# Performance work log

Hardware: AMD Instinct MI355X
Metric: run time of the kernel (lower is better)

Reference implementation:

```python
import jax, jax.numpy as jnp
import numpy as np

OUT, IN, RANK = 4096, 4096, 256
SUBVEC = 8
N_SUBVECS = OUT * RANK // SUBVEC  # 131072 (same for Vh since IN == OUT here)
NNZ = 262144


def setup_inputs() -> dict:
    key = jax.random.key(0)
    ks = jax.random.split(key, 8)
    x = jax.random.normal(ks[0], (4, 128, IN), dtype=jnp.float32)
    U_indices = jax.random.randint(ks[1], (N_SUBVECS,), 0, 256, dtype=jnp.int32)
    U_codebook = jax.random.normal(ks[2], (256, SUBVEC), dtype=jnp.float32)
    S = jax.random.uniform(ks[3], (RANK,), dtype=jnp.float32)
    Vh_indices = jax.random.randint(ks[4], (N_SUBVECS,), 0, 256, dtype=jnp.int32)
    Vh_codebook = jax.random.normal(ks[5], (256, SUBVEC), dtype=jnp.float32)
    residual_indices = jax.random.randint(ks[6], (NNZ,), 0, OUT * IN, dtype=jnp.int32)
    residual_values = jax.random.normal(ks[7], (NNZ,), dtype=jnp.float32)
    return {
        "x": x,
        "U_indices": U_indices,
        "U_codebook": U_codebook,
        "S": S,
        "Vh_indices": Vh_indices,
        "Vh_codebook": Vh_codebook,
        "residual_indices": residual_indices,
        "residual_values": residual_values,
    }


def reference(x, U_indices, U_codebook, S, Vh_indices, Vh_codebook,
              residual_indices, residual_values):
    # Codebook gather -> flatten -> reshape to factor shape (dims divide evenly,
    # so torch's flat[:n] truncation is a no-op here).
    U = U_codebook[U_indices].reshape(OUT, RANK)      # [out, rank]
    Vh = Vh_codebook[Vh_indices].reshape(RANK, IN)    # [rank, in]
    # U @ diag(S) @ Vh, fused as column-scale of U
    weight = (U * S[None, :]) @ Vh                    # [out, in]
    # sparse residual scatter-add into the flat weight
    weight = weight.reshape(-1).at[residual_indices].add(residual_values)
    weight = weight.reshape(OUT, IN)
    # F.linear(x, weight) == x @ weight.T (bias is None)
    return jnp.einsum("bsi,oi->bso", x, weight)
```

## Files before the change

### kernel.cpp

```cpp
#include <hip/hip_runtime.h>
#include <hip/hip_bf16.h>
#include <stdint.h>

#define IN_DIM   4096
#define OUT_DIM  4096
#define RANK     256
#define MROWS    512
#define NNZ_CNT  262144
#define BCAP     128
#define CSTRIDE  16

typedef __attribute__((ext_vector_type(8))) short bf16x8;
typedef __attribute__((ext_vector_type(4))) float f32x4;

#define WS_VHB  ((size_t)0)
#define WS_USB  (WS_VHB + (size_t)RANK * IN_DIM * 2)
#define WS_XT   (WS_USB + (size_t)OUT_DIM * RANK * 2)
#define WS_T    (WS_XT  + (size_t)IN_DIM * MROWS * 2)
#define WS_CUR  (WS_T   + (size_t)MROWS * RANK * 4)
#define WS_KVB  (WS_CUR + (size_t)OUT_DIM * CSTRIDE * 4)

__device__ inline uint4 pack8(float4 a, float4 b) {
    union { __hip_bfloat16 h[8]; uint4 u; } w;
    w.h[0] = __float2bfloat16(a.x); w.h[1] = __float2bfloat16(a.y);
    w.h[2] = __float2bfloat16(a.z); w.h[3] = __float2bfloat16(a.w);
    w.h[4] = __float2bfloat16(b.x); w.h[5] = __float2bfloat16(b.y);
    w.h[6] = __float2bfloat16(b.z); w.h[7] = __float2bfloat16(b.w);
    return w.u;
}

__device__ inline float bfbits(uint32_t lo16) {
    union { uint32_t u; float f; } w; w.u = lo16 << 16; return w.f;
}

__device__ inline void fma8(float* acc, uint4 u, float v) {
    acc[0] += v * bfbits(u.x & 0xffffu);
    acc[1] += v * bfbits(u.x >> 16);
    acc[2] += v * bfbits(u.y & 0xffffu);
    acc[3] += v * bfbits(u.y >> 16);
    acc[4] += v * bfbits(u.z & 0xffffu);
    acc[5] += v * bfbits(u.z >> 16);
    acc[6] += v * bfbits(u.w & 0xffffu);
    acc[7] += v * bfbits(u.w >> 16);
}

__global__ __launch_bounds__(256) void prep_kernel(
    const float* __restrict__ x,
    const int*   __restrict__ uidx, const float* __restrict__ ucode,
    const float* __restrict__ S,
    const int*   __restrict__ vidx, const float* __restrict__ vcode,
    __hip_bfloat16* __restrict__ Vhb, __hip_bfloat16* __restrict__ Usb,
    __hip_bfloat16* __restrict__ xT,
    int* __restrict__ cursor, float* __restrict__ tbuf)
{
    const int bid = blockIdx.x;
    const int t   = threadIdx.x;

    if (bid < 512) {
        __shared__ float tile[64][65];
        const int i0 = (bid >> 3) * 64;
        const int m0 = (bid & 7) * 64;
        const int rr = t >> 4, c4 = t & 15;
        #pragma unroll
        for (int p = 0; p < 4; p++) {
            int r = p * 16 + rr;
            float4 v = *(const float4*)(x + (size_t)(m0 + r) * IN_DIM + i0 + c4 * 4);
            tile[r][c4 * 4 + 0] = v.x;
            tile[r][c4 * 4 + 1] = v.y;
            tile[r][c4 * 4 + 2] = v.z;
            tile[r][c4 * 4 + 3] = v.w;
        }
        tbuf[bid * 256 + t] = 0.f;
        __syncthreads();
        #pragma unroll
        for (int p = 0; p < 4; p++) {
            int i = p * 16 + rr;
            union { __hip_bfloat16 h[4]; uint2 u; } w;
            w.h[0] = __float2bfloat16(tile[c4 * 4 + 0][i]);
            w.h[1] = __float2bfloat16(tile[c4 * 4 + 1][i]);
            w.h[2] = __float2bfloat16(tile[c4 * 4 + 2][i]);
            w.h[3] = __float2bfloat16(tile[c4 * 4 + 3][i]);
            *(uint2*)(xT + (size_t)(i0 + i) * MROWS + m0 + c4 * 4) = w.u;
        }
    } else if (bid < 768) {
        int base = (bid - 512) * 512;
        #pragma unroll
        for (int q = 0; q < 2; q++) {
            int sv = base + q * 256 + t;
            int cb = vidx[sv];
            const float4* vc = (const float4*)(vcode + (size_t)cb * 8);
            *(uint4*)(Vhb + (size_t)sv * 8) = pack8(vc[0], vc[1]);
        }
    } else {
        int base = (bid - 768) * 512;
        #pragma unroll
        for (int q = 0; q < 2; q++) {
            int sv = base + q * 256 + t;
            int cb = uidx[sv];
            int r0 = (sv & 31) * 8;
            const float4* uc = (const float4*)(ucode + (size_t)cb * 8);
            const float4* sp = (const float4*)(S + r0);
            float4 a = uc[0], b = uc[1], sa = sp[0], sb = sp[1];
            a.x *= sa.x; a.y *= sa.y; a.z *= sa.z; a.w *= sa.w;
            b.x *= sb.x; b.y *= sb.y; b.z *= sb.z; b.w *= sb.w;
            *(uint4*)(Usb + (size_t)sv * 8) = pack8(a, b);
        }
        cursor[(bid - 768) * 256 + t] = 0;
    }
}

__global__ __launch_bounds__(256) void scatter_gemm1_kernel(
    const int* __restrict__ ridx, const float* __restrict__ rval,
    int* __restrict__ cursor, int2* __restrict__ kvb,
    const float* __restrict__ x,
    const __hip_bfloat16* __restrict__ Vhb,
    float* __restrict__ tbuf)
{
    if (blockIdx.x < 1024) {
        int k = blockIdx.x * 256 + threadIdx.x;
        int idx = ridx[k];
        int o = idx >> 12, i = idx & 4095;
        int pos = atomicAdd(&cursor[o * CSTRIDE], 1);
        if (pos < BCAP)
            kvb[(size_t)o * BCAP + pos] = make_int2(i, __float_as_int(rval[k]));
        return;
    }

    __shared__ __align__(16) __hip_bfloat16 As[64][72];
    __shared__ __align__(16) __hip_bfloat16 Bs[64][72];

    const int bid = blockIdx.x - 1024;
    const int ks = bid & 7, nb = (bid >> 3) & 3, mb = bid >> 5;
    const int m0 = mb * 64, n0 = nb * 64, kbase = ks * 512;
    const int t = threadIdx.x;
    const int lane = t & 63, wave = t >> 6;
    const int wm = wave >> 1, wn = wave & 1;
    const int l15 = lane & 15, l4 = lane >> 4;
    const int srow = t >> 2, sg = t & 3;

    f32x4 acc[2][2];
    #pragma unroll
    for (int i = 0; i < 2; i++)
        #pragma unroll
        for (int j = 0; j < 2; j++) acc[i][j] = (f32x4){0.f, 0.f, 0.f, 0.f};

    for (int s = 0; s < 8; s++) {
        int k0 = kbase + s * 64;
        const float* xp = x + (size_t)(m0 + srow) * IN_DIM + k0 + sg * 16;
        *(uint4*)&As[srow][sg * 16] =
            pack8(*(const float4*)xp, *(const float4*)(xp + 4));
        *(uint4*)&As[srow][sg * 16 + 8] =
            pack8(*(const float4*)(xp + 8), *(const float4*)(xp + 12));
        const __hip_bfloat16* bp = Vhb + (size_t)(n0 + srow) * IN_DIM + k0 + sg * 16;
        *(uint4*)&Bs[srow][sg * 16]     = *(const uint4*)bp;
        *(uint4*)&Bs[srow][sg * 16 + 8] = *(const uint4*)(bp + 8);
        __syncthreads();
        #pragma unroll
        for (int kk = 0; kk < 2; kk++) {
            bf16x8 a[2], b[2];
            #pragma unroll
            for (int i = 0; i < 2; i++)
                a[i] = *(const bf16x8*)&As[wm * 32 + i * 16 + l15][kk * 32 + l4 * 8];
            #pragma unroll
            for (int j = 0; j < 2; j++)
                b[j] = *(const bf16x8*)&Bs[wn * 32 + j * 16 + l15][kk * 32 + l4 * 8];
            #pragma unroll
            for (int i = 0; i < 2; i++)
                #pragma unroll
                for (int j = 0; j < 2; j++)
                    acc[i][j] = __builtin_amdgcn_mfma_f32_16x16x32_bf16(
                        a[i], b[j], acc[i][j], 0, 0, 0);
        }
        __syncthreads();
    }

    #pragma unroll
    for (int i = 0; i < 2; i++)
        #pragma unroll
        for (int j = 0; j < 2; j++)
            #pragma unroll
            for (int q = 0; q < 4; q++) {
                int row = m0 + wm * 32 + i * 16 + l4 * 4 + q;
                int col = n0 + wn * 32 + j * 16 + l15;
                atomicAdd(&tbuf[row * RANK + col], acc[i][j][q]);
            }
}

__global__ __launch_bounds__(256) void gemm2_sparse_kernel(
    const float* __restrict__ tbuf,
    const __hip_bfloat16* __restrict__ Usb,
    const int* __restrict__ cursor,
    const int2* __restrict__ kvb,
    const __hip_bfloat16* __restrict__ xT,
    float* __restrict__ out)
{
    __shared__ __align__(16) char smem[14080];
    typedef __hip_bfloat16 bfrowA[72];
    typedef __hip_bfloat16 bfrowB[72];
    bfrowA* As = (bfrowA*)smem;
    bfrowB* Bs = (bfrowB*)(smem + 4608);
    float (*sacc)[33] = (float(*)[33])smem;

    const int bid = blockIdx.x;
    const int mb = bid & 15, nb = bid >> 4;
    const int m0 = mb * 32, n0 = nb * 64;
    const int t = threadIdx.x;
    const int lane = t & 63, wave = t >> 6;
    const int wm = wave >> 1, wn = wave & 1;
    const int l15 = lane & 15, l4 = lane >> 4;

    f32x4 acc[2];
    acc[0] = (f32x4){0.f, 0.f, 0.f, 0.f};
    acc[1] = (f32x4){0.f, 0.f, 0.f, 0.f};

    {
        const int sa_row = t >> 3, sa_g = t & 7;
        const int sb_row = t >> 2, sb_g = t & 3;
        for (int s = 0; s < 4; s++) {
            int k0 = s * 64;
            const float* tp = tbuf + (size_t)(m0 + sa_row) * RANK + k0 + sa_g * 8;
            *(uint4*)&As[sa_row][sa_g * 8] =
                pack8(*(const float4*)tp, *(const float4*)(tp + 4));
            const __hip_bfloat16* bp =
                Usb + (size_t)(n0 + sb_row) * RANK + k0 + sb_g * 16;
            *(uint4*)&Bs[sb_row][sb_g * 16]     = *(const uint4*)bp;
            *(uint4*)&Bs[sb_row][sb_g * 16 + 8] = *(const uint4*)(bp + 8);
            __syncthreads();
            #pragma unroll
            for (int kk = 0; kk < 2; kk++) {
                bf16x8 a, b[2];
                a = *(const bf16x8*)&As[wm * 16 + l15][kk * 32 + l4 * 8];
                #pragma unroll
                for (int j = 0; j < 2; j++)
                    b[j] = *(const bf16x8*)&Bs[wn * 32 + j * 16 + l15][kk * 32 + l4 * 8];
                #pragma unroll
                for (int j = 0; j < 2; j++)
                    acc[j] = __builtin_amdgcn_mfma_f32_16x16x32_bf16(
                        a, b[j], acc[j], 0, 0, 0);
            }
            __syncthreads();
        }
    }

    {
        const int orel = t >> 2;
        const int ms   = t & 3;
        const int o    = n0 + orel;
        int cnt = cursor[o * CSTRIDE]; cnt = cnt < BCAP ? cnt : BCAP;
        const int2* kp  = kvb + (size_t)o * BCAP;
        const int4* kp4 = (const int4*)kp;
        const __hip_bfloat16* xm = xT + m0 + ms * 8;

        float r[8];
        #pragma unroll
        for (int j = 0; j < 8; j++) r[j] = 0.f;

        int k = 0;
        for (; k + 8 <= cnt; k += 8) {
            int4 e0 = kp4[(k >> 1) + 0], e1 = kp4[(k >> 1) + 1];
            int4 e2 = kp4[(k >> 1) + 2], e3 = kp4[(k >> 1) + 3];
            uint4 u0 = *(const uint4*)(xm + (size_t)e0.x * MROWS);
            uint4 u1 = *(const uint4*)(xm + (size_t)e0.z * MROWS);
            uint4 u2 = *(const uint4*)(xm + (size_t)e1.x * MROWS);
            uint4 u3 = *(const uint4*)(xm + (size_t)e1.z * MROWS);
            uint4 u4 = *(const uint4*)(xm + (size_t)e2.x * MROWS);
            uint4 u5 = *(const uint4*)(xm + (size_t)e2.z * MROWS);
            uint4 u6 = *(const uint4*)(xm + (size_t)e3.x * MROWS);
            uint4 u7 = *(const uint4*)(xm + (size_t)e3.z * MROWS);
            fma8(r, u0, __int_as_float(e0.y));
            fma8(r, u1, __int_as_float(e0.w));
            fma8(r, u2, __int_as_float(e1.y));
            fma8(r, u3, __int_as_float(e1.w));
            fma8(r, u4, __int_as_float(e2.y));
            fma8(r, u5, __int_as_float(e2.w));
            fma8(r, u6, __int_as_float(e3.y));
            fma8(r, u7, __int_as_float(e3.w));
        }
        if (k + 4 <= cnt) {
            int4 e0 = kp4[(k >> 1) + 0], e1 = kp4[(k >> 1) + 1];
            uint4 u0 = *(const uint4*)(xm + (size_t)e0.x * MROWS);
            uint4 u1 = *(const uint4*)(xm + (size_t)e0.z * MROWS);
            uint4 u2 = *(const uint4*)(xm + (size_t)e1.x * MROWS);
            uint4 u3 = *(const uint4*)(xm + (size_t)e1.z * MROWS);
            fma8(r, u0, __int_as_float(e0.y));
            fma8(r, u1, __int_as_float(e0.w));
            fma8(r, u2, __int_as_float(e1.y));
            fma8(r, u3, __int_as_float(e1.w));
            k += 4;
        }
        for (; k < cnt; k++) {
            int2 e = kp[k];
            uint4 u = *(const uint4*)(xm + (size_t)e.x * MROWS);
            fma8(r, u, __int_as_float(e.y));
        }

        *(float4*)&sacc[orel][ms * 8]     = make_float4(r[0], r[1], r[2], r[3]);
        *(float4*)&sacc[orel][ms * 8 + 4] = make_float4(r[4], r[5], r[6], r[7]);
    }
    __syncthreads();

    #pragma unroll
    for (int j = 0; j < 2; j++)
        #pragma unroll
        for (int q = 0; q < 4; q++) {
            int rrel = wm * 16 + l4 * 4 + q;
            int crel = wn * 32 + j * 16 + l15;
            out[(size_t)(m0 + rrel) * OUT_DIM + n0 + crel] =
                acc[j][q] + sacc[crel][rrel];
        }
}

extern "C" void kernel_launch(void* const* d_in, const int* in_sizes, int n_in,
                              void* d_out, int out_size, void* d_ws, size_t ws_size,
                              hipStream_t stream)
{
    const float* x    = (const float*)d_in[0];
    const int*   uidx = (const int*)  d_in[1];
    const float* ucb  = (const float*)d_in[2];
    const float* S    = (const float*)d_in[3];
    const int*   vidx = (const int*)  d_in[4];
    const float* vcb  = (const float*)d_in[5];
    const int*   ridx = (const int*)  d_in[6];
    const float* rval = (const float*)d_in[7];
    float* out = (float*)d_out;

    char* ws = (char*)d_ws;
    __hip_bfloat16* Vhb  = (__hip_bfloat16*)(ws + WS_VHB);
    __hip_bfloat16* Usb  = (__hip_bfloat16*)(ws + WS_USB);
    __hip_bfloat16* xT   = (__hip_bfloat16*)(ws + WS_XT);
    float*          tbuf = (float*)(ws + WS_T);
    int*            cur  = (int*)(ws + WS_CUR);
    int2*           kvb  = (int2*)(ws + WS_KVB);

    prep_kernel<<<dim3(1024), dim3(256), 0, stream>>>(
        x, uidx, ucb, S, vidx, vcb, Vhb, Usb, xT, cur, tbuf);

    scatter_gemm1_kernel<<<dim3(1280), dim3(256), 0, stream>>>(
        ridx, rval, cur, kvb, x, Vhb, tbuf);

    gemm2_sparse_kernel<<<dim3(1024), dim3(256), 0, stream>>>(
        tbuf, Usb, cur, kvb, xT, out);
}
```

Before: 62.69 us.

## Double gemm2 block threads, split sparse nonzero lists across two halves

The gemm2_sparse kernel moves from 256 to 512 threads per block. The A and B tile loads are split between the two halves of the block, and each wave now computes one 16x16 MFMA tile instead of two. Each output column's sparse residual list is split between two threads whose partial sums are combined through an enlarged shared-memory buffer. This aims to raise parallelism and memory-level concurrency in the latency-bound sparse gather, at the cost of more shared memory, more threads and shorter unrolled gather loops.

Result: slower. 65.29 us (+4.2%).

```diff
diff --git a/kernel.cpp b/kernel.cpp
--- a/kernel.cpp
+++ b/kernel.cpp
@@ -186,7 +186,7 @@
             }
 }
 
-__global__ __launch_bounds__(256) void gemm2_sparse_kernel(
+__global__ __launch_bounds__(512, 8) void gemm2_sparse_kernel(
     const float* __restrict__ tbuf,
     const __hip_bfloat16* __restrict__ Usb,
     const int* __restrict__ cursor,
@@ -194,59 +194,58 @@
     const __hip_bfloat16* __restrict__ xT,
     float* __restrict__ out)
 {
-    __shared__ __align__(16) char smem[14080];
+    __shared__ __align__(16) char smem[16896];
     typedef __hip_bfloat16 bfrowA[72];
     typedef __hip_bfloat16 bfrowB[72];
     bfrowA* As = (bfrowA*)smem;
     bfrowB* Bs = (bfrowB*)(smem + 4608);
-    float (*sacc)[33] = (float(*)[33])smem;
+    float (*sacc2)[64][33] = (float(*)[64][33])smem;
 
     const int bid = blockIdx.x;
     const int mb = bid & 15, nb = bid >> 4;
     const int m0 = mb * 32, n0 = nb * 64;
     const int t = threadIdx.x;
     const int lane = t & 63, wave = t >> 6;
-    const int wm = wave >> 1, wn = wave & 1;
+    const int wm = wave >> 2, wn = wave & 3;
     const int l15 = lane & 15, l4 = lane >> 4;
 
-    f32x4 acc[2];
-    acc[0] = (f32x4){0.f, 0.f, 0.f, 0.f};
-    acc[1] = (f32x4){0.f, 0.f, 0.f, 0.f};
+    f32x4 acc = (f32x4){0.f, 0.f, 0.f, 0.f};
+
+    for (int s = 0; s < 4; s++) {
+        int k0 = s * 64;
+        if (t < 256) {
+            int row = t >> 3, g = t & 7;
+            const float* tp = tbuf + (size_t)(m0 + row) * RANK + k0 + g * 8;
+            *(uint4*)&As[row][g * 8] =
+                pack8(*(const float4*)tp, *(const float4*)(tp + 4));
+        } else {
+            int tt = t - 256;
+            int row = tt >> 2, g = tt & 3;
+            const __hip_bfloat16* bp =
+                Usb + (size_t)(n0 + row) * RANK + k0 + g * 16;
+            *(uint4*)&Bs[row][g * 16]     = *(const uint4*)bp;
+            *(uint4*)&Bs[row][g * 16 + 8] = *(const uint4*)(bp + 8);
+        }
+        __syncthreads();
+        #pragma unroll
+        for (int kk = 0; kk < 2; kk++) {
+            bf16x8 a = *(const bf16x8*)&As[wm * 16 + l15][kk * 32 + l4 * 8];
+            bf16x8 b = *(const bf16x8*)&Bs[wn * 16 + l15][kk * 32 + l4 * 8];
+            acc = __builtin_amdgcn_mfma_f32_16x16x32_bf16(a, b, acc, 0, 0, 0);
+        }
+        __syncthreads();
+    }
 
     {
-        const int sa_row = t >> 3, sa_g = t & 7;
-        const int sb_row = t >> 2, sb_g = t & 3;
-        for (int s = 0; s < 4; s++) {
-            int k0 = s * 64;
-            const float* tp = tbuf + (size_t)(m0 + sa_row) * RANK + k0 + sa_g * 8;
-            *(uint4*)&As[sa_row][sa_g * 8] =
-                pack8(*(const float4*)tp, *(const float4*)(tp + 4));
-            const __hip_bfloat16* bp =
-                Usb + (size_t)(n0 + sb_row) * RANK + k0 + sb_g * 16;
-            *(uint4*)&Bs[sb_row][sb_g * 16]     = *(const uint4*)bp;
-            *(uint4*)&Bs[sb_row][sb_g * 16 + 8] = *(const uint4*)(bp + 8);
-            __syncthreads();
-            #pragma unroll
-            for (int kk = 0; kk < 2; kk++) {
-                bf16x8 a, b[2];
-                a = *(const bf16x8*)&As[wm * 16 + l15][kk * 32 + l4 * 8];
-                #pragma unroll
-                for (int j = 0; j < 2; j++)
-                    b[j] = *(const bf16x8*)&Bs[wn * 32 + j * 16 + l15][kk * 32 + l4 * 8];
-                #pragma unroll
-                for (int j = 0; j < 2; j++)
-                    acc[j] = __builtin_amdgcn_mfma_f32_16x16x32_bf16(
-                        a, b[j], acc[j], 0, 0, 0);
-            }
-            __syncthreads();
-        }
-    }
-
-    {
-        const int orel = t >> 2;
-        const int ms   = t & 3;
+        const int orel = t >> 3;
+        const int sub  = t & 7;
+        const int ms   = sub & 3;
+        const int h    = sub >> 2;
         const int o    = n0 + orel;
         int cnt = cursor[o * CSTRIDE]; cnt = cnt < BCAP ? cnt : BCAP;
+        const int mid = (cnt >> 1) & ~1;
+        const int kb = h ? mid : 0;
+        const int ke = h ? cnt : mid;
         const int2* kp  = kvb + (size_t)o * BCAP;
         const int4* kp4 = (const int4*)kp;
         const __hip_bfloat16* xm = xT + m0 + ms * 8;
@@ -255,28 +254,8 @@
         #pragma unroll
         for (int j = 0; j < 8; j++) r[j] = 0.f;
 
-        int k = 0;
-        for (; k + 8 <= cnt; k += 8) {
-            int4 e0 = kp4[(k >> 1) + 0], e1 = kp4[(k >> 1) + 1];
-            int4 e2 = kp4[(k >> 1) + 2], e3 = kp4[(k >> 1) + 3];
-            uint4 u0 = *(const uint4*)(xm + (size_t)e0.x * MROWS);
-            uint4 u1 = *(const uint4*)(xm + (size_t)e0.z * MROWS);
-            uint4 u2 = *(const uint4*)(xm + (size_t)e1.x * MROWS);
-            uint4 u3 = *(const uint4*)(xm + (size_t)e1.z * MROWS);
-            uint4 u4 = *(const uint4*)(xm + (size_t)e2.x * MROWS);
-            uint4 u5 = *(const uint4*)(xm + (size_t)e2.z * MROWS);
-            uint4 u6 = *(const uint4*)(xm + (size_t)e3.x * MROWS);
-            uint4 u7 = *(const uint4*)(xm + (size_t)e3.z * MROWS);
-            fma8(r, u0, __int_as_float(e0.y));
-            fma8(r, u1, __int_as_float(e0.w));
-            fma8(r, u2, __int_as_float(e1.y));
-            fma8(r, u3, __int_as_float(e1.w));
-            fma8(r, u4, __int_as_float(e2.y));
-            fma8(r, u5, __int_as_float(e2.w));
-            fma8(r, u6, __int_as_float(e3.y));
-            fma8(r, u7, __int_as_float(e3.w));
-        }
-        if (k + 4 <= cnt) {
+        int k = kb;
+        for (; k + 4 <= ke; k += 4) {
             int4 e0 = kp4[(k >> 1) + 0], e1 = kp4[(k >> 1) + 1];
             uint4 u0 = *(const uint4*)(xm + (size_t)e0.x * MROWS);
             uint4 u1 = *(const uint4*)(xm + (size_t)e0.z * MROWS);
@@ -286,28 +265,33 @@
             fma8(r, u1, __int_as_float(e0.w));
             fma8(r, u2, __int_as_float(e1.y));
             fma8(r, u3, __int_as_float(e1.w));
-            k += 4;
-        }
-        for (; k < cnt; k++) {
+        }
+        if (k + 2 <= ke) {
+            int4 e0 = kp4[k >> 1];
+            uint4 u0 = *(const uint4*)(xm + (size_t)e0.x * MROWS);
+            uint4 u1 = *(const uint4*)(xm + (size_t)e0.z * MROWS);
+            fma8(r, u0, __int_as_float(e0.y));
+            fma8(r, u1, __int_as_float(e0.w));
+            k += 2;
+        }
+        if (k < ke) {
             int2 e = kp[k];
             uint4 u = *(const uint4*)(xm + (size_t)e.x * MROWS);
             fma8(r, u, __int_as_float(e.y));
         }
 
-        *(float4*)&sacc[orel][ms * 8]     = make_float4(r[0], r[1], r[2], r[3]);
-        *(float4*)&sacc[orel][ms * 8 + 4] = make_float4(r[4], r[5], r[6], r[7]);
+        *(float4*)&sacc2[h][orel][ms * 8]     = make_float4(r[0], r[1], r[2], r[3]);
+        *(float4*)&sacc2[h][orel][ms * 8 + 4] = make_float4(r[4], r[5], r[6], r[7]);
     }
     __syncthreads();
 
     #pragma unroll
-    for (int j = 0; j < 2; j++)
-        #pragma unroll
-        for (int q = 0; q < 4; q++) {
-            int rrel = wm * 16 + l4 * 4 + q;
-            int crel = wn * 32 + j * 16 + l15;
-            out[(size_t)(m0 + rrel) * OUT_DIM + n0 + crel] =
-                acc[j][q] + sacc[crel][rrel];
-        }
+    for (int q = 0; q < 4; q++) {
+        int rrel = wm * 16 + l4 * 4 + q;
+        int crel = wn * 16 + l15;
+        out[(size_t)(m0 + rrel) * OUT_DIM + n0 + crel] =
+            acc[q] + sacc2[0][crel][rrel] + sacc2[1][crel][rrel];
+    }
 }
 
 extern "C" void kernel_launch(void* const* d_in, const int* in_sizes, int n_in,
@@ -338,6 +322,6 @@
     scatter_gemm1_kernel<<<dim3(1280), dim3(256), 0, stream>>>(
         ridx, rval, cur, kvb, x, Vhb, tbuf);
 
-    gemm2_sparse_kernel<<<dim3(1024), dim3(256), 0, stream>>>(
+    gemm2_sparse_kernel<<<dim3(1024), dim3(512), 0, stream>>>(
         tbuf, Usb, cur, kvb, xT, out);
 }
```

## Move x transpose into middle kernel and schedule GEMM1 blocks first

Applied to the files above, without the earlier changes.

The x-to-bf16 transpose moves out of the prep kernel into the middle kernel, where it runs alongside the residual scatter and the first low-rank GEMM. GEMM1 blocks get the lowest block indices so the long-running MFMA work is dispatched first and the scatter and transpose blocks fill in behind it. The prep kernel shrinks to codebook decoding plus zeroing of tbuf and the cursors. This rebalances work across the kernel stages to shorten the critical path, at the cost of a larger middle launch with shared-memory use that varies by block role.

After: 62.75 us. No clear change (+0.1%).

```diff
diff --git a/kernel.cpp b/kernel.cpp
--- a/kernel.cpp
+++ b/kernel.cpp
@@ -45,45 +45,17 @@
 }
 
 __global__ __launch_bounds__(256) void prep_kernel(
-    const float* __restrict__ x,
     const int*   __restrict__ uidx, const float* __restrict__ ucode,
     const float* __restrict__ S,
     const int*   __restrict__ vidx, const float* __restrict__ vcode,
     __hip_bfloat16* __restrict__ Vhb, __hip_bfloat16* __restrict__ Usb,
-    __hip_bfloat16* __restrict__ xT,
     int* __restrict__ cursor, float* __restrict__ tbuf)
 {
     const int bid = blockIdx.x;
     const int t   = threadIdx.x;
 
-    if (bid < 512) {
-        __shared__ float tile[64][65];
-        const int i0 = (bid >> 3) * 64;
-        const int m0 = (bid & 7) * 64;
-        const int rr = t >> 4, c4 = t & 15;
-        #pragma unroll
-        for (int p = 0; p < 4; p++) {
-            int r = p * 16 + rr;
-            float4 v = *(const float4*)(x + (size_t)(m0 + r) * IN_DIM + i0 + c4 * 4);
-            tile[r][c4 * 4 + 0] = v.x;
-            tile[r][c4 * 4 + 1] = v.y;
-            tile[r][c4 * 4 + 2] = v.z;
-            tile[r][c4 * 4 + 3] = v.w;
-        }
-        tbuf[bid * 256 + t] = 0.f;
-        __syncthreads();
-        #pragma unroll
-        for (int p = 0; p < 4; p++) {
-            int i = p * 16 + rr;
-            union { __hip_bfloat16 h[4]; uint2 u; } w;
-            w.h[0] = __float2bfloat16(tile[c4 * 4 + 0][i]);
-            w.h[1] = __float2bfloat16(tile[c4 * 4 + 1][i]);
-            w.h[2] = __float2bfloat16(tile[c4 * 4 + 2][i]);
-            w.h[3] = __float2bfloat16(tile[c4 * 4 + 3][i]);
-            *(uint2*)(xT + (size_t)(i0 + i) * MROWS + m0 + c4 * 4) = w.u;
-        }
-    } else if (bid < 768) {
-        int base = (bid - 512) * 512;
+    if (bid < 256) {
+        int base = bid * 512;
         #pragma unroll
         for (int q = 0; q < 2; q++) {
             int sv = base + q * 256 + t;
@@ -92,7 +64,7 @@
             *(uint4*)(Vhb + (size_t)sv * 8) = pack8(vc[0], vc[1]);
         }
     } else {
-        int base = (bid - 768) * 512;
+        int base = (bid - 256) * 512;
         #pragma unroll
         for (int q = 0; q < 2; q++) {
             int sv = base + q * 256 + t;
@@ -105,85 +77,116 @@
             b.x *= sb.x; b.y *= sb.y; b.z *= sb.z; b.w *= sb.w;
             *(uint4*)(Usb + (size_t)sv * 8) = pack8(a, b);
         }
-        cursor[(bid - 768) * 256 + t] = 0;
+        cursor[(bid - 256) * 256 + t] = 0;
     }
-}
-
-__global__ __launch_bounds__(256) void scatter_gemm1_kernel(
+    tbuf[bid * 256 + t] = 0.f;
+}
+
+__global__ __launch_bounds__(256) void mid_kernel(
     const int* __restrict__ ridx, const float* __restrict__ rval,
     int* __restrict__ cursor, int2* __restrict__ kvb,
     const float* __restrict__ x,
     const __hip_bfloat16* __restrict__ Vhb,
-    float* __restrict__ tbuf)
+    float* __restrict__ tbuf,
+    __hip_bfloat16* __restrict__ xT)
 {
-    if (blockIdx.x < 1024) {
-        int k = blockIdx.x * 256 + threadIdx.x;
+    __shared__ __align__(16) char smem[18432];
+    const int t = threadIdx.x;
+
+    if (blockIdx.x < 256) {
+        typedef __hip_bfloat16 bfrow[72];
+        bfrow* As = (bfrow*)smem;
+        bfrow* Bs = (bfrow*)(smem + 9216);
+
+        const int bid = blockIdx.x;
+        const int ks = bid & 7, nb = (bid >> 3) & 3, mb = bid >> 5;
+        const int m0 = mb * 64, n0 = nb * 64, kbase = ks * 512;
+        const int lane = t & 63, wave = t >> 6;
+        const int wm = wave >> 1, wn = wave & 1;
+        const int l15 = lane & 15, l4 = lane >> 4;
+        const int srow = t >> 2, sg = t & 3;
+
+        f32x4 acc[2][2];
+        #pragma unroll
+        for (int i = 0; i < 2; i++)
+            #pragma unroll
+            for (int j = 0; j < 2; j++) acc[i][j] = (f32x4){0.f, 0.f, 0.f, 0.f};
+
+        for (int s = 0; s < 8; s++) {
+            int k0 = kbase + s * 64;
+            const float* xp = x + (size_t)(m0 + srow) * IN_DIM + k0 + sg * 16;
+            *(uint4*)&As[srow][sg * 16] =
+                pack8(*(const float4*)xp, *(const float4*)(xp + 4));
+            *(uint4*)&As[srow][sg * 16 + 8] =
+                pack8(*(const float4*)(xp + 8), *(const float4*)(xp + 12));
+            const __hip_bfloat16* bp =
+                Vhb + (size_t)(n0 + srow) * IN_DIM + k0 + sg * 16;
+            *(uint4*)&Bs[srow][sg * 16]     = *(const uint4*)bp;
+            *(uint4*)&Bs[srow][sg * 16 + 8] = *(const uint4*)(bp + 8);
+            __syncthreads();
+            #pragma unroll
+            for (int kk = 0; kk < 2; kk++) {
+                bf16x8 a[2], b[2];
+                #pragma unroll
+                for (int i = 0; i < 2; i++)
+                    a[i] = *(const bf16x8*)&As[wm * 32 + i * 16 + l15][kk * 32 + l4 * 8];
+                #pragma unroll
+                for (int j = 0; j < 2; j++)
+                    b[j] = *(const bf16x8*)&Bs[wn * 32 + j * 16 + l15][kk * 32 + l4 * 8];
+                #pragma unroll
+                for (int i = 0; i < 2; i++)
+                    #pragma unroll
+                    for (int j = 0; j < 2; j++)
+                        acc[i][j] = __builtin_amdgcn_mfma_f32_16x16x32_bf16(
+                            a[i], b[j], acc[i][j], 0, 0, 0);
+            }
+            __syncthreads();
+        }
+
+        #pragma unroll
+        for (int i = 0; i < 2; i++)
+            #pragma unroll
+            for (int j = 0; j < 2; j++)
+                #pragma unroll
+                for (int q = 0; q < 4; q++) {
+                    int row = m0 + wm * 32 + i * 16 + l4 * 4 + q;
+                    int col = n0 + wn * 32 + j * 16 + l15;
+                    atomicAdd(&tbuf[row * RANK + col], acc[i][j][q]);
+                }
+    } else if (blockIdx.x < 1280) {
+        int k = (blockIdx.x - 256) * 256 + t;
         int idx = ridx[k];
         int o = idx >> 12, i = idx & 4095;
         int pos = atomicAdd(&cursor[o * CSTRIDE], 1);
         if (pos < BCAP)
             kvb[(size_t)o * BCAP + pos] = make_int2(i, __float_as_int(rval[k]));
-        return;
+    } else {
+        float (*tile)[65] = (float(*)[65])smem;
+        const int tb = blockIdx.x - 1280;
+        const int i0 = (tb >> 3) * 64;
+        const int m0 = (tb & 7) * 64;
+        const int rr = t >> 4, c4 = t & 15;
+        #pragma unroll
+        for (int p = 0; p < 4; p++) {
+            int r = p * 16 + rr;
+            float4 v = *(const float4*)(x + (size_t)(m0 + r) * IN_DIM + i0 + c4 * 4);
+            tile[r][c4 * 4 + 0] = v.x;
+            tile[r][c4 * 4 + 1] = v.y;
+            tile[r][c4 * 4 + 2] = v.z;
+            tile[r][c4 * 4 + 3] = v.w;
+        }
+        __syncthreads();
+        #pragma unroll
+        for (int p = 0; p < 4; p++) {
+            int i = p * 16 + rr;
+            union { __hip_bfloat16 h[4]; uint2 u; } w;
+            w.h[0] = __float2bfloat16(tile[c4 * 4 + 0][i]);
+            w.h[1] = __float2bfloat16(tile[c4 * 4 + 1][i]);
+            w.h[2] = __float2bfloat16(tile[c4 * 4 + 2][i]);
+            w.h[3] = __float2bfloat16(tile[c4 * 4 + 3][i]);
+            *(uint2*)(xT + (size_t)(i0 + i) * MROWS + m0 + c4 * 4) = w.u;
+        }
     }
-
-    __shared__ __align__(16) __hip_bfloat16 As[64][72];
-    __shared__ __align__(16) __hip_bfloat16 Bs[64][72];
-
-    const int bid = blockIdx.x - 1024;
-    const int ks = bid & 7, nb = (bid >> 3) & 3, mb = bid >> 5;
-    const int m0 = mb * 64, n0 = nb * 64, kbase = ks * 512;
-    const int t = threadIdx.x;
-    const int lane = t & 63, wave = t >> 6;
-    const int wm = wave >> 1, wn = wave & 1;
-    const int l15 = lane & 15, l4 = lane >> 4;
-    const int srow = t >> 2, sg = t & 3;
-
-    f32x4 acc[2][2];
-    #pragma unroll
-    for (int i = 0; i < 2; i++)
-        #pragma unroll
-        for (int j = 0; j < 2; j++) acc[i][j] = (f32x4){0.f, 0.f, 0.f, 0.f};
-
-    for (int s = 0; s < 8; s++) {
-        int k0 = kbase + s * 64;
-        const float* xp = x + (size_t)(m0 + srow) * IN_DIM + k0 + sg * 16;
-        *(uint4*)&As[srow][sg * 16] =
-            pack8(*(const float4*)xp, *(const float4*)(xp + 4));
-        *(uint4*)&As[srow][sg * 16 + 8] =
-            pack8(*(const float4*)(xp + 8), *(const float4*)(xp + 12));
-        const __hip_bfloat16* bp = Vhb + (size_t)(n0 + srow) * IN_DIM + k0 + sg * 16;
-        *(uint4*)&Bs[srow][sg * 16]     = *(const uint4*)bp;
-        *(uint4*)&Bs[srow][sg * 16 + 8] = *(const uint4*)(bp + 8);
-        __syncthreads();
-        #pragma unroll
-        for (int kk = 0; kk < 2; kk++) {
-            bf16x8 a[2], b[2];
-            #pragma unroll
-            for (int i = 0; i < 2; i++)
-                a[i] = *(const bf16x8*)&As[wm * 32 + i * 16 + l15][kk * 32 + l4 * 8];
-            #pragma unroll
-            for (int j = 0; j < 2; j++)
-                b[j] = *(const bf16x8*)&Bs[wn * 32 + j * 16 + l15][kk * 32 + l4 * 8];
-            #pragma unroll
-            for (int i = 0; i < 2; i++)
-                #pragma unroll
-                for (int j = 0; j < 2; j++)
-                    acc[i][j] = __builtin_amdgcn_mfma_f32_16x16x32_bf16(
-                        a[i], b[j], acc[i][j], 0, 0, 0);
-        }
-        __syncthreads();
-    }
-
-    #pragma unroll
-    for (int i = 0; i < 2; i++)
-        #pragma unroll
-        for (int j = 0; j < 2; j++)
-            #pragma unroll
-            for (int q = 0; q < 4; q++) {
-                int row = m0 + wm * 32 + i * 16 + l4 * 4 + q;
-                int col = n0 + wn * 32 + j * 16 + l15;
-                atomicAdd(&tbuf[row * RANK + col], acc[i][j][q]);
-            }
 }
 
 __global__ __launch_bounds__(256) void gemm2_sparse_kernel(
@@ -332,11 +335,11 @@
     int*            cur  = (int*)(ws + WS_CUR);
     int2*           kvb  = (int2*)(ws + WS_KVB);
 
-    prep_kernel<<<dim3(1024), dim3(256), 0, stream>>>(
-        x, uidx, ucb, S, vidx, vcb, Vhb, Usb, xT, cur, tbuf);
-
-    scatter_gemm1_kernel<<<dim3(1280), dim3(256), 0, stream>>>(
-        ridx, rval, cur, kvb, x, Vhb, tbuf);
+    prep_kernel<<<dim3(512), dim3(256), 0, stream>>>(
+        uidx, ucb, S, vidx, vcb, Vhb, Usb, cur, tbuf);
+
+    mid_kernel<<<dim3(1792), dim3(256), 0, stream>>>(
+        ridx, rval, cur, kvb, x, Vhb, tbuf, xT);
 
     gemm2_sparse_kernel<<<dim3(1024), dim3(256), 0, stream>>>(
         tbuf, Usb, cur, kvb, xT, out);
```
